# Performance work log

Hardware: AMD Instinct MI355X
Metric: run time of the kernel (lower is better)

The kernel has to match this reference:

```python
import jax, jax.numpy as jnp
import numpy as np

ALPHA = 30.0  # init kwarg alpha
K = 16        # init kwarg k


def setup_inputs() -> dict:
    key = jax.random.key(0)
    k1, k2 = jax.random.split(key)
    x = jax.random.normal(k1, (4096, 1024), dtype=jnp.float32)
    # L2-normalize embeddings (standard for metric-learning losses) so
    # pairwise distances lie in [0, 2] and exp(alpha*(1-d)) is well-scaled.
    x = x / jnp.linalg.norm(x, axis=1, keepdims=True)
    t = jax.random.randint(k2, (4096,), 0, 64)
    return {"inputs": x, "targets": t}


def _knn_softmax(inputs, targets):
    n = inputs.shape[0]
    # pairwise euclidean distances, clamp(1e-12).sqrt as in euclidean_dist
    sq = jnp.sum(inputs * inputs, axis=1)
    dist = sq[:, None] + sq[None, :] - 2.0 * (inputs @ inputs.T)
    dist = jnp.sqrt(jnp.clip(dist, 1e-12))  # [n, n]

    eye = jnp.eye(n, dtype=bool)
    same = targets[:, None] == targets[None, :]
    pos_mask = same & ~eye        # same label, off-diagonal
    neg_mask = ~same              # different label (diag excluded automatically)

    # threshold = (K+1)-th smallest off-diagonal distance per row
    # (equals sorted(concat(pos_pair, neg_pair))[K] in the original)
    BIG = jnp.float32(1e30)
    thr = jnp.sort(jnp.where(eye, BIG, dist), axis=1)[:, K]  # [n]

    below = dist < thr[:, None]
    logits = jnp.exp(ALPHA * (1.0 - dist))  # exp(alpha*(1 - d)) per pair

    pos_below = pos_mask & below
    neg_below = neg_mask & below
    pos_logit = jnp.sum(jnp.where(pos_below, logits, 0.0), axis=1)
    neg_logit = jnp.sum(jnp.where(neg_below, logits, 0.0), axis=1)

    # fallback: if no positive neighbor below threshold, use the first
    # positive pair (masked_select returns row order -> smallest index)
    first_pos = jnp.argmax(pos_mask, axis=1)
    fb = jnp.take_along_axis(logits, first_pos[:, None], axis=1)[:, 0]
    has_pos_below = jnp.any(pos_below, axis=1)
    pos_logit = jnp.where(has_pos_below, pos_logit, fb)

    loss_i = -jnp.log(pos_logit / (pos_logit + neg_logit))  # [n]

    # rows with no positive or no negative pair are skipped in the original
    valid = jnp.any(pos_mask, axis=1) & jnp.any(neg_mask, axis=1)
    n_valid = jnp.sum(valid.astype(jnp.float32))
    loss = jnp.sum(jnp.where(valid, loss_i, 0.0)) / n_valid
    accuracy = jnp.sum((valid & (loss_i < 0.6)).astype(jnp.float32)) / n
    return loss, accuracy


def reference(inputs, targets):
    loss, accuracy = _knn_softmax(inputs, targets)
    return (loss, accuracy, 0.0, 0.0)
```

## Files before the change

kernel.cpp:

```cpp
#include <hip/hip_runtime.h>
#include <hip/hip_bf16.h>
#include <cfloat>
#include <climits>
#include <cstdint>

#define ALPHA 30.0f
#define KSEL 16
#define P0 1.368f
#define P0SQ (P0 * P0)
#define CAP 224
#define TCAP 512
#define BIGV 1e30f
#define NMAX 4096

typedef __attribute__((ext_vector_type(4))) float f32x4;
typedef __attribute__((ext_vector_type(8))) int i32x8;
typedef __attribute__((ext_vector_type(4))) int i32x4;

#define LDS_PTR(p) ((__attribute__((address_space(3))) uint32_t*)(p))
#define GLB_PTR(p) ((const __attribute__((address_space(1))) uint32_t*)(p))

__device__ inline float bfval(ushort u) {
    return __builtin_bit_cast(float, (uint32_t)u << 16);
}

__device__ inline float blockReduceSumF(float v, float* s) {
    for (int off = 32; off; off >>= 1) v += __shfl_down(v, off);
    int tid = threadIdx.x, wid = tid >> 6;
    if ((tid & 63) == 0) s[wid] = v;
    __syncthreads();
    float r;
    if (tid == 0) { r = s[0] + s[1] + s[2] + s[3]; s[0] = r; }
    __syncthreads();
    r = s[0];
    __syncthreads();
    return r;
}

__device__ inline int blockReduceSumI(int v, int* s) {
    for (int off = 32; off; off >>= 1) v += __shfl_down(v, off);
    int tid = threadIdx.x, wid = tid >> 6;
    if ((tid & 63) == 0) s[wid] = v;
    __syncthreads();
    int r;
    if (tid == 0) { r = s[0] + s[1] + s[2] + s[3]; s[0] = r; }
    __syncthreads();
    r = s[0];
    __syncthreads();
    return r;
}

__device__ inline int blockReduceMaxI(int v, int* s) {
    for (int off = 32; off; off >>= 1) v = max(v, __shfl_down(v, off));
    int tid = threadIdx.x, wid = tid >> 6;
    if ((tid & 63) == 0) s[wid] = v;
    __syncthreads();
    int r;
    if (tid == 0) { r = max(max(s[0], s[1]), max(s[2], s[3])); s[0] = r; }
    __syncthreads();
    r = s[0];
    __syncthreads();
    return r;
}

__global__ __launch_bounds__(256) void prep_kernel(const float* __restrict__ X,
                                                   ushort* __restrict__ Xbf,
                                                   uint32_t* __restrict__ Xb8,
                                                   float* __restrict__ sq,
                                                   const int* __restrict__ targets,
                                                   int* __restrict__ f1,
                                                   int* __restrict__ f2,
                                                   int* __restrict__ lcnt,
                                                   int D, int N) {
    __shared__ float sw[4];
    __shared__ int s1[4], s2[4], sc[4];
    int tid = threadIdx.x;
    int wid = tid >> 6;

    if (blockIdx.x >= (unsigned)N) {
        int lbl = blockIdx.x - N;
        int a1 = INT_MAX, a2 = INT_MAX, c = 0;
        for (int j = tid; j < N; j += 256) {
            if (targets[j] == lbl) {
                ++c;
                if (j < a1) { a2 = a1; a1 = j; }
                else if (j < a2) a2 = j;
            }
        }
        for (int off = 32; off; off >>= 1) {
            int b1 = __shfl_down(a1, off), b2 = __shfl_down(a2, off), bc = __shfl_down(c, off);
            int m1 = min(a1, b1);
            int m2 = min(max(a1, b1), min(a2, b2));
            a1 = m1; a2 = m2; c += bc;
        }
        if ((tid & 63) == 0) { s1[wid] = a1; s2[wid] = a2; sc[wid] = c; }
        __syncthreads();
        if (tid == 0) {
            int r1 = s1[0], r2 = s2[0], rc = sc[0];
            for (int w = 1; w < 4; ++w) {
                int m1 = min(r1, s1[w]);
                int m2 = min(max(r1, s1[w]), min(r2, s2[w]));
                r1 = m1; r2 = m2; rc += sc[w];
            }
            f1[lbl] = r1; f2[lbl] = r2; lcnt[lbl] = rc;
        }
        return;
    }

    int row = blockIdx.x;
    const float4* xr = reinterpret_cast<const float4*>(X + (size_t)row * D);
    ushort4* xo = reinterpret_cast<ushort4*>(Xbf + (size_t)row * D);
    uint32_t* x8o = Xb8 + (size_t)row * (D / 4);
    float s = 0.f;
    for (int c = tid; c < D / 4; c += 256) {
        float4 v = xr[c];
        s += v.x * v.x + v.y * v.y + v.z * v.z + v.w * v.w;
        ushort4 o;
        uint32_t b;
        b = __builtin_bit_cast(uint32_t, v.x); o.x = (ushort)((b + 0x7FFF + ((b >> 16) & 1)) >> 16);
        b = __builtin_bit_cast(uint32_t, v.y); o.y = (ushort)((b + 0x7FFF + ((b >> 16) & 1)) >> 16);
        b = __builtin_bit_cast(uint32_t, v.z); o.z = (ushort)((b + 0x7FFF + ((b >> 16) & 1)) >> 16);
        b = __builtin_bit_cast(uint32_t, v.w); o.w = (ushort)((b + 0x7FFF + ((b >> 16) & 1)) >> 16);
        xo[c] = o;
        int pk = __builtin_amdgcn_cvt_pk_fp8_f32(v.x * 16.f, v.y * 16.f, 0, false);
        pk = __builtin_amdgcn_cvt_pk_fp8_f32(v.z * 16.f, v.w * 16.f, pk, true);
        x8o[c] = (uint32_t)pk;
    }
    for (int off = 32; off; off >>= 1) s += __shfl_down(s, off);
    if ((tid & 63) == 0) sw[wid] = s;
    __syncthreads();
    if (tid == 0) sq[row] = sw[0] + sw[1] + sw[2] + sw[3];
}

#define GBM 128
#define GBK 128
__global__ __launch_bounds__(256) void distgemm_mfma(const uint8_t* __restrict__ Xb8,
                                                     const float* __restrict__ sq,
                                                     float2* __restrict__ cand,
                                                     int* __restrict__ cntArr,
                                                     int* __restrict__ needFB,
                                                     int N, int D) {
    if (blockIdx.x < blockIdx.y) return;
    __shared__ uint8_t As[GBM * GBK];
    __shared__ uint8_t Bs[GBM * GBK];
    __shared__ float2 tlist[TCAP];
    __shared__ int s_cnt;

    int by = blockIdx.y, bx = blockIdx.x;
    bool diag = (bx == by);

    int tid = threadIdx.x;
    int lane = tid & 63;
    int wave = tid >> 6;
    int waveR = wave >> 1;
    int waveC = wave & 1;

    int rowBase = by * GBM;
    int colBase = bx * GBM;

    if (tid == 0) s_cnt = 0;

    f32x4 acc[4][4];
#pragma unroll
    for (int m = 0; m < 4; ++m)
#pragma unroll
        for (int n2 = 0; n2 < 4; ++n2) {
            f32x4 z = {0.f, 0.f, 0.f, 0.f};
            acc[m][n2] = z;
        }

    int srow = lane >> 3;
    int sgb = ((lane & 7) << 4) ^ (srow << 4);
    auto STAGE = [&](int k0) {
#pragma unroll
        for (int p = 0; p < 4; ++p) {
            int c = wave * 4 + p;
            int r = c * 8 + srow;
            const uint8_t* gA = Xb8 + (size_t)(rowBase + r) * D + k0 + sgb;
            const uint8_t* gB = Xb8 + (size_t)(colBase + r) * D + k0 + sgb;
            __builtin_amdgcn_global_load_lds(GLB_PTR(gA), LDS_PTR(&As[c * 1024]), 16, 0, 0);
            __builtin_amdgcn_global_load_lds(GLB_PTR(gB), LDS_PTR(&Bs[c * 1024]), 16, 0, 0);
        }
    };

    int l15 = lane & 15;
    int kq32 = (lane >> 4) * 32;
    int rswz = (l15 & 7) << 4;
    int nt = D / GBK;

    for (int t = 0; t < nt; ++t) {
        STAGE(t * GBK);
        __syncthreads();

        i32x8 bF[4];
#pragma unroll
        for (int n2 = 0; n2 < 4; ++n2) {
            int brl = waveC * 64 + n2 * 16 + l15;
            const uint8_t* base = Bs + brl * 128;
            i32x4 lo = *reinterpret_cast<const i32x4*>(base + ((kq32) ^ rswz));
            i32x4 hi = *reinterpret_cast<const i32x4*>(base + ((kq32 + 16) ^ rswz));
            i32x8 f = {lo[0], lo[1], lo[2], lo[3], hi[0], hi[1], hi[2], hi[3]};
            bF[n2] = f;
        }
        __builtin_amdgcn_s_setprio(1);
#pragma unroll
        for (int m = 0; m < 4; ++m) {
            int arl = waveR * 64 + m * 16 + l15;
            const uint8_t* base = As + arl * 128;
            i32x4 lo = *reinterpret_cast<const i32x4*>(base + ((kq32) ^ rswz));
            i32x4 hi = *reinterpret_cast<const i32x4*>(base + ((kq32 + 16) ^ rswz));
            i32x8 aF = {lo[0], lo[1], lo[2], lo[3], hi[0], hi[1], hi[2], hi[3]};
#pragma unroll
            for (int n2 = 0; n2 < 4; ++n2)
                acc[m][n2] = __builtin_amdgcn_mfma_scale_f32_16x16x128_f8f6f4(
                    aF, bF[n2], acc[m][n2], 0, 0, 0, 0x7F, 0, 0x7F);
        }
        __builtin_amdgcn_s_setprio(0);
        __syncthreads();
    }

    int cr = (lane >> 4) * 4;
    int cc = lane & 15;
    unsigned long long lmask_lt = (1ull << lane) - 1ull;
#pragma unroll
    for (int m = 0; m < 4; ++m) {
#pragma unroll
        for (int n2 = 0; n2 < 4; ++n2) {
            int gcol = colBase + waveC * 64 + n2 * 16 + cc;
            float sqc = sq[gcol];
#pragma unroll
            for (int r = 0; r < 4; ++r) {
                int grow = rowBase + waveR * 64 + m * 16 + cr + r;
                float v = sq[grow] + sqc - acc[m][n2][r] * 0.0078125f;
                bool pred = (v < P0SQ) && (grow != gcol);
                unsigned long long mask = __ballot(pred);
                if (mask) {
                    int leader = __ffsll((long long)mask) - 1;
                    int tot = __popcll(mask);
                    int base = 0;
                    if (lane == leader) base = atomicAdd(&s_cnt, tot);
                    base = __shfl(base, leader);
                    if (pred) {
                        int idx = base + __popcll(mask & lmask_lt);
                        if (idx < TCAP) {
                            float d = sqrtf(fmaxf(v, 1e-12f));
                            uint32_t pk = ((uint32_t)grow << 12) | (uint32_t)gcol;
                            float2 e; e.x = d; e.y = __builtin_bit_cast(float, pk);
                            tlist[idx] = e;
                        }
                    }
                }
            }
        }
    }
    __syncthreads();

    int cnt = min(s_cnt, TCAP);
    for (int e = tid; e < cnt; e += 256) {
        float2 v = tlist[e];
        uint32_t pk = __builtin_bit_cast(uint32_t, v.y);
        int i = (int)(pk >> 12), j = (int)(pk & 4095u);
        int p = atomicAdd(&cntArr[i], 1);
        if (p < CAP) {
            float2 e1; e1.x = v.x; e1.y = __builtin_bit_cast(float, j);
            cand[(size_t)i * CAP + p] = e1;
        }
        if (!diag) {
            int q = atomicAdd(&cntArr[j], 1);
            if (q < CAP) {
                float2 e2; e2.x = v.x; e2.y = __builtin_bit_cast(float, i);
                cand[(size_t)j * CAP + q] = e2;
            }
        }
    }
    if (s_cnt > TCAP) {
        if (tid < GBM) needFB[rowBase + tid] = 1;
        else needFB[colBase + tid - GBM] = 1;
    }
}

__global__ __launch_bounds__(256) void rowfinal_kernel(const float2* __restrict__ cand,
                                                       const int* __restrict__ cntArr,
                                                       const int* __restrict__ targets,
                                                       const ushort* __restrict__ Xbf,
                                                       const float* __restrict__ sq,
                                                       const int* __restrict__ f1,
                                                       const int* __restrict__ f2,
                                                       const int* __restrict__ lcnt,
                                                       int* __restrict__ needFB,
                                                       float* __restrict__ rowLoss,
                                                       int N, int D) {
    __shared__ float dbuf[4][CAP];
    int tid = threadIdx.x, lane = tid & 63, w = tid >> 6;
    int row = blockIdx.x * 4 + w;
    int ti = targets[row];
    int lc = lcnt[ti];
    bool validRow = (lc >= 2) && (lc < N);
    int cnt = cntArr[row];
    bool fb = (cnt < KSEL + 1) || (cnt > CAP);
    int lim = fb ? 0 : cnt;

    float ed[4]; int ej[4];
#pragma unroll
    for (int s = 0; s < 4; ++s) {
        int idx = lane + s * 64;
        bool in = (!fb) && (idx < cnt);
        if (in) {
            float2 e = cand[(size_t)row * CAP + idx];
            ed[s] = e.x; ej[s] = __builtin_bit_cast(int, e.y);
            dbuf[w][idx] = e.x;
        } else { ed[s] = BIGV; ej[s] = -1; }
    }
    __syncthreads();

    int rlo[4] = {0, 0, 0, 0}, req[4] = {0, 0, 0, 0};
    for (int q = 0; q < lim; ++q) {
        float u = dbuf[w][q];
#pragma unroll
        for (int s = 0; s < 4; ++s) {
            rlo[s] += (u < ed[s]);
            req[s] += (u == ed[s]);
        }
    }
    float thrc = BIGV;
#pragma unroll
    for (int s = 0; s < 4; ++s)
        if (ej[s] >= 0 && rlo[s] <= KSEL && KSEL < rlo[s] + req[s]) thrc = fminf(thrc, ed[s]);
    for (int off = 32; off; off >>= 1) thrc = fminf(thrc, __shfl_down(thrc, off));
    float thr = __shfl(thrc, 0);

    float posS = 0.f, negS = 0.f;
    int apb = 0;
#pragma unroll
    for (int s = 0; s < 4; ++s) {
        if (ej[s] >= 0 && ed[s] < thr) {
            bool same = (targets[ej[s]] == ti);
            float e = expf(ALPHA * (1.0f - ed[s]));
            if (same) { posS += e; apb = 1; }
            else negS += e;
        }
    }
    for (int off = 32; off; off >>= 1) {
        posS += __shfl_down(posS, off);
        negS += __shfl_down(negS, off);
        apb = max(apb, __shfl_down(apb, off));
    }

    int fp = 0;
    float dot = 0.f;
    if (validRow) {
        fp = (row == f1[ti]) ? f2[ti] : f1[ti];
        const ushort* xr = Xbf + (size_t)row * D;
        const ushort* xf = Xbf + (size_t)fp * D;
        for (int c = lane; c < D / 4; c += 64) {
            ushort4 a = *reinterpret_cast<const ushort4*>(xr + (size_t)c * 4);
            ushort4 b = *reinterpret_cast<const ushort4*>(xf + (size_t)c * 4);
            dot += bfval(a.x) * bfval(b.x) + bfval(a.y) * bfval(b.y)
                 + bfval(a.z) * bfval(b.z) + bfval(a.w) * bfval(b.w);
        }
    }
    for (int off = 32; off; off >>= 1) dot += __shfl_down(dot, off);

    if (lane == 0) {
        if (fb) {
            needFB[row] = 1;
        } else if (!validRow) {
            rowLoss[row] = BIGV;
        } else {
            float fbD = sqrtf(fmaxf(sq[row] + sq[fp] - 2.0f * dot, 1e-12f));
            float posLogit = apb ? posS : expf(ALPHA * (1.0f - fbD));
            rowLoss[row] = -logf(posLogit / (posLogit + negS));
        }
    }
}

__global__ __launch_bounds__(256) void fallback_kernel(const ushort* __restrict__ Xbf,
                                                       const float* __restrict__ sq,
                                                       const int* __restrict__ targets,
                                                       const int* __restrict__ needFB,
                                                       const int* __restrict__ f1,
                                                       const int* __restrict__ f2,
                                                       const int* __restrict__ lcnt,
                                                       float* __restrict__ rowLoss,
                                                       int N, int D) {
    int row = blockIdx.x;
    if (!needFB[row]) return;

    __shared__ float xrow[1024];
    __shared__ float rowD[NMAX];
    __shared__ float sF[4];
    __shared__ int sI[4];
    int tid = threadIdx.x;

    for (int k = tid; k < D; k += 256) xrow[k] = bfval(Xbf[(size_t)row * D + k]);
    __syncthreads();

    for (int j = tid; j < N; j += 256) {
        float dot = 0.f;
        const ushort* xj = Xbf + (size_t)j * D;
        for (int k = 0; k < D; ++k) dot += xrow[k] * bfval(xj[k]);
        rowD[j] = (j == row) ? BIGV
                             : sqrtf(fmaxf(sq[row] + sq[j] - 2.0f * dot, 1e-12f));
    }
    __syncthreads();

    uint32_t lo = 0, hi = 0x40800000u;
    while (lo < hi) {
        uint32_t mid = (lo + hi) >> 1;
        float mv = __builtin_bit_cast(float, mid);
        int c = 0;
        for (int j = tid; j < N; j += 256) c += (rowD[j] <= mv);
        c = blockReduceSumI(c, sI);
        if (c >= KSEL + 1) hi = mid; else lo = mid + 1;
    }
    float thr = __builtin_bit_cast(float, hi);

    int ti = targets[row];
    int lc = lcnt[ti];
    bool validRow = (lc >= 2) && (lc < N);

    float posS = 0.f, negS = 0.f;
    int apb = 0;
    for (int j = tid; j < N; j += 256) {
        if (j == row) continue;
        float d = rowD[j];
        bool same = (targets[j] == ti);
        if (d < thr) {
            float e = expf(ALPHA * (1.0f - d));
            if (same) { posS += e; apb = 1; }
            else negS += e;
        }
    }
    posS = blockReduceSumF(posS, sF);
    negS = blockReduceSumF(negS, sF);
    apb = blockReduceMaxI(apb, sI);

    if (tid == 0) {
        if (!validRow) { rowLoss[row] = BIGV; return; }
        int fp = (row == f1[ti]) ? f2[ti] : f1[ti];
        float posLogit = apb ? posS : expf(ALPHA * (1.0f - rowD[fp]));
        rowLoss[row] = -logf(posLogit / (posLogit + negS));
    }
}

__global__ __launch_bounds__(256) void reduce_kernel(const float* __restrict__ rowLoss,
                                                     float* __restrict__ out, int N) {
    __shared__ float sF[4];
    __shared__ int sI[4];
    int tid = threadIdx.x;
    float sumL = 0.f;
    int nValid = 0, nAcc = 0;
    for (int j = tid; j < N; j += 256) {
        float L = rowLoss[j];
        if (L != BIGV) {
            sumL += L;
            ++nValid;
            if (L < 0.6f) ++nAcc;
        }
    }
    sumL = blockReduceSumF(sumL, sF);
    nValid = blockReduceSumI(nValid, sI);
    nAcc = blockReduceSumI(nAcc, sI);
    if (tid == 0) {
        out[0] = (nValid > 0) ? sumL / (float)nValid : 0.f;
        out[1] = (float)nAcc / (float)N;
        out[2] = 0.f;
        out[3] = 0.f;
    }
}

extern "C" void kernel_launch(void* const* d_in, const int* in_sizes, int n_in,
                              void* d_out, int out_size, void* d_ws, size_t ws_size,
                              hipStream_t stream) {
    const float* X = (const float*)d_in[0];
    const int* targets = (const int*)d_in[1];
    float* out = (float*)d_out;

    int N = in_sizes[1];
    int D = in_sizes[0] / N;
    int tiles = N / GBM;

    float2* cand     = (float2*)d_ws;
    float*  sq       = (float*)(cand + (size_t)N * CAP);
    float*  rowLoss  = sq + N;
    int*    cntArr   = (int*)(rowLoss + N);
    int*    needFB   = cntArr + N;
    int*    f1       = needFB + N;
    int*    f2       = f1 + 64;
    int*    lcnt     = f2 + 64;
    ushort* Xbf      = (ushort*)(lcnt + 64 + 64);
    uint32_t* Xb8    = (uint32_t*)(Xbf + (size_t)N * D);

    hipMemsetAsync(cntArr, 0, N * sizeof(int), stream);
    hipMemsetAsync(needFB, 0, N * sizeof(int), stream);

    prep_kernel<<<N + 64, 256, 0, stream>>>(X, Xbf, Xb8, sq, targets,
                                            f1, f2, lcnt, D, N);

    dim3 grid(tiles, tiles);
    distgemm_mfma<<<grid, 256, 0, stream>>>((const uint8_t*)Xb8, sq, cand,
                                            cntArr, needFB, N, D);

    rowfinal_kernel<<<N / 4, 256, 0, stream>>>(cand, cntArr, targets, Xbf, sq,
                                               f1, f2, lcnt, needFB, rowLoss, N, D);

    fallback_kernel<<<N, 256, 0, stream>>>(Xbf, sq, targets, needFB,
                                           f1, f2, lcnt, rowLoss, N, D);

    reduce_kernel<<<1, 256, 0, stream>>>(rowLoss, out, N);
}
```

Measured before the change: 113.3 us.

## Use full square grid of 256x256 tiles with XCD-aware block remap

Replaces the upper-triangular 128x128 tile grid, which used symmetric scatter, with a full 16x16 grid of 256x256 tiles run by 512-thread blocks. Each wave now computes a 128x64 sub-tile. Block IDs are remapped across the 8 XCDs, and each tile writes candidates only for its own rows, which removes the mirrored atomics. The aim is more reuse per tile loaded into LDS and the removal of idle triangular blocks, at the cost of computing the whole matrix twice. It also raises LDS use and leaves only 256 blocks, which lowers occupancy.

Measured after the change: 127.9 us. +12.9%, slower.

```diff
diff --git a/kernel.cpp b/kernel.cpp
--- a/kernel.cpp
+++ b/kernel.cpp
@@ -9,7 +9,7 @@
 #define P0 1.368f
 #define P0SQ (P0 * P0)
 #define CAP 224
-#define TCAP 512
+#define TCAP 1664
 #define BIGV 1e30f
 #define NMAX 4096
 
@@ -132,37 +132,37 @@
     if (tid == 0) sq[row] = sw[0] + sw[1] + sw[2] + sw[3];
 }
 
-#define GBM 128
+#define GBM 256
 #define GBK 128
-__global__ __launch_bounds__(256) void distgemm_mfma(const uint8_t* __restrict__ Xb8,
+__global__ __launch_bounds__(512) void distgemm_mfma(const uint8_t* __restrict__ Xb8,
                                                      const float* __restrict__ sq,
                                                      float2* __restrict__ cand,
                                                      int* __restrict__ cntArr,
                                                      int* __restrict__ needFB,
                                                      int N, int D) {
-    if (blockIdx.x < blockIdx.y) return;
     __shared__ uint8_t As[GBM * GBK];
     __shared__ uint8_t Bs[GBM * GBK];
     __shared__ float2 tlist[TCAP];
     __shared__ int s_cnt;
 
-    int by = blockIdx.y, bx = blockIdx.x;
-    bool diag = (bx == by);
+    int wg = blockIdx.x;
+    int wgid = (wg & 7) * 32 + (wg >> 3);
+    int by = wgid >> 4, bx = wgid & 15;
 
     int tid = threadIdx.x;
     int lane = tid & 63;
     int wave = tid >> 6;
-    int waveR = wave >> 1;
-    int waveC = wave & 1;
+    int waveM = wave >> 2;
+    int waveN = wave & 3;
 
     int rowBase = by * GBM;
     int colBase = bx * GBM;
 
     if (tid == 0) s_cnt = 0;
 
-    f32x4 acc[4][4];
-#pragma unroll
-    for (int m = 0; m < 4; ++m)
+    f32x4 acc[8][4];
+#pragma unroll
+    for (int m = 0; m < 8; ++m)
 #pragma unroll
         for (int n2 = 0; n2 < 4; ++n2) {
             f32x4 z = {0.f, 0.f, 0.f, 0.f};
@@ -174,12 +174,13 @@
     auto STAGE = [&](int k0) {
 #pragma unroll
         for (int p = 0; p < 4; ++p) {
-            int c = wave * 4 + p;
-            int r = c * 8 + srow;
+            int r = p * 64 + wave * 8 + srow;
             const uint8_t* gA = Xb8 + (size_t)(rowBase + r) * D + k0 + sgb;
             const uint8_t* gB = Xb8 + (size_t)(colBase + r) * D + k0 + sgb;
-            __builtin_amdgcn_global_load_lds(GLB_PTR(gA), LDS_PTR(&As[c * 1024]), 16, 0, 0);
-            __builtin_amdgcn_global_load_lds(GLB_PTR(gB), LDS_PTR(&Bs[c * 1024]), 16, 0, 0);
+            uint8_t* dA = &As[p * 8192 + wave * 1024];
+            uint8_t* dB = &Bs[p * 8192 + wave * 1024];
+            __builtin_amdgcn_global_load_lds(GLB_PTR(gA), LDS_PTR(dA), 16, 0, 0);
+            __builtin_amdgcn_global_load_lds(GLB_PTR(gB), LDS_PTR(dB), 16, 0, 0);
         }
     };
 
@@ -195,7 +196,7 @@
         i32x8 bF[4];
 #pragma unroll
         for (int n2 = 0; n2 < 4; ++n2) {
-            int brl = waveC * 64 + n2 * 16 + l15;
+            int brl = waveN * 64 + n2 * 16 + l15;
             const uint8_t* base = Bs + brl * 128;
             i32x4 lo = *reinterpret_cast<const i32x4*>(base + ((kq32) ^ rswz));
             i32x4 hi = *reinterpret_cast<const i32x4*>(base + ((kq32 + 16) ^ rswz));
@@ -204,8 +205,8 @@
         }
         __builtin_amdgcn_s_setprio(1);
 #pragma unroll
-        for (int m = 0; m < 4; ++m) {
-            int arl = waveR * 64 + m * 16 + l15;
+        for (int m = 0; m < 8; ++m) {
+            int arl = waveM * 128 + m * 16 + l15;
             const uint8_t* base = As + arl * 128;
             i32x4 lo = *reinterpret_cast<const i32x4*>(base + ((kq32) ^ rswz));
             i32x4 hi = *reinterpret_cast<const i32x4*>(base + ((kq32 + 16) ^ rswz));
@@ -223,14 +224,14 @@
     int cc = lane & 15;
     unsigned long long lmask_lt = (1ull << lane) - 1ull;
 #pragma unroll
-    for (int m = 0; m < 4; ++m) {
+    for (int m = 0; m < 8; ++m) {
 #pragma unroll
         for (int n2 = 0; n2 < 4; ++n2) {
-            int gcol = colBase + waveC * 64 + n2 * 16 + cc;
+            int gcol = colBase + waveN * 64 + n2 * 16 + cc;
             float sqc = sq[gcol];
 #pragma unroll
             for (int r = 0; r < 4; ++r) {
-                int grow = rowBase + waveR * 64 + m * 16 + cr + r;
+                int grow = rowBase + waveM * 128 + m * 16 + cr + r;
                 float v = sq[grow] + sqc - acc[m][n2][r] * 0.0078125f;
                 bool pred = (v < P0SQ) && (grow != gcol);
                 unsigned long long mask = __ballot(pred);
@@ -256,7 +257,7 @@
     __syncthreads();
 
     int cnt = min(s_cnt, TCAP);
-    for (int e = tid; e < cnt; e += 256) {
+    for (int e = tid; e < cnt; e += 512) {
         float2 v = tlist[e];
         uint32_t pk = __builtin_bit_cast(uint32_t, v.y);
         int i = (int)(pk >> 12), j = (int)(pk & 4095u);
@@ -265,18 +266,9 @@
             float2 e1; e1.x = v.x; e1.y = __builtin_bit_cast(float, j);
             cand[(size_t)i * CAP + p] = e1;
         }
-        if (!diag) {
-            int q = atomicAdd(&cntArr[j], 1);
-            if (q < CAP) {
-                float2 e2; e2.x = v.x; e2.y = __builtin_bit_cast(float, i);
-                cand[(size_t)j * CAP + q] = e2;
-            }
-        }
-    }
-    if (s_cnt > TCAP) {
-        if (tid < GBM) needFB[rowBase + tid] = 1;
-        else needFB[colBase + tid - GBM] = 1;
-    }
+    }
+    if (s_cnt > TCAP && tid < GBM)
+        needFB[rowBase + tid] = 1;
 }
 
 __global__ __launch_bounds__(256) void rowfinal_kernel(const float2* __restrict__ cand,
@@ -479,6 +471,7 @@
     int N = in_sizes[1];
     int D = in_sizes[0] / N;
     int tiles = N / GBM;
+    int nTiles = tiles * tiles;
 
     float2* cand     = (float2*)d_ws;
     float*  sq       = (float*)(cand + (size_t)N * CAP);
@@ -497,9 +490,8 @@
     prep_kernel<<<N + 64, 256, 0, stream>>>(X, Xbf, Xb8, sq, targets,
                                             f1, f2, lcnt, D, N);
 
-    dim3 grid(tiles, tiles);
-    distgemm_mfma<<<grid, 256, 0, stream>>>((const uint8_t*)Xb8, sq, cand,
-                                            cntArr, needFB, N, D);
+    distgemm_mfma<<<nTiles, 512, 0, stream>>>((const uint8_t*)Xb8, sq, cand,
+                                              cntArr, needFB, N, D);
 
     rowfinal_kernel<<<N / 4, 256, 0, stream>>>(cand, cntArr, targets, Xbf, sq,
                                                f1, f2, lcnt, needFB, rowLoss, N, D);
```
